# Optimization experiments

Measured on AMD Instinct MI355X. Metric: run time of the kernel, lower is better.

Reference implementation:

```python
import jax, jax.numpy as jnp
import numpy as np

N_HEAD = 12

def setup_inputs() -> dict:
    key = jax.random.key(0)
    k1, k2, k3, k4, k5 = jax.random.split(key, 5)
    B, T, C = 2, 2048, 768
    x = jax.random.normal(k1, (B, T, C), dtype=jnp.float32)
    W_attn = jax.random.normal(k2, (C, 3 * C), dtype=jnp.float32) * 0.02
    b_attn = jax.random.normal(k3, (3 * C,), dtype=jnp.float32) * 0.02
    W_proj = jax.random.normal(k4, (C, C), dtype=jnp.float32) * 0.02
    b_proj = jax.random.normal(k5, (C,), dtype=jnp.float32) * 0.02
    return {"x": x, "W_attn": W_attn, "b_attn": b_attn, "W_proj": W_proj, "b_proj": b_proj}

def reference(x, W_attn, b_attn, W_proj, b_proj):
    B, T, C = x.shape
    H = N_HEAD
    hd = C // H
    qkv = x @ W_attn + b_attn  # [B,T,3C]
    q, k, v = jnp.split(qkv, 3, axis=2)
    # [B,H,T,hd]
    q = q.reshape(B, T, H, hd).transpose(0, 2, 1, 3)
    k = k.reshape(B, T, H, hd).transpose(0, 2, 1, 3)
    v = v.reshape(B, T, H, hd).transpose(0, 2, 1, 3)
    att = jnp.einsum('bhqd,bhkd->bhqk', q, k) / jnp.sqrt(jnp.float32(hd))
    causal = jnp.tril(jnp.ones((T, T), dtype=bool))
    att = jnp.where(causal[None, None], att, -jnp.inf)
    att = jax.nn.softmax(att, axis=-1)
    y = jnp.einsum('bhqk,bhkd->bhqd', att, v)  # [B,H,T,hd]
    y = y.transpose(0, 2, 1, 3).reshape(B, T, C)
    return y @ W_proj + b_proj
```

## Files before the change

### kernel.cpp

```cpp
#include <hip/hip_runtime.h>
#include <stdint.h>

typedef unsigned short u16;
typedef __attribute__((ext_vector_type(8))) short bf16x8;
typedef __attribute__((ext_vector_type(4))) float f32x4;

__device__ __forceinline__ u16 f2bf(float f){
  union { float f; uint32_t u; } v; v.f = f;
  uint32_t u = v.u;
  u += 0x7FFFu + ((u >> 16) & 1u);
  return (u16)(u >> 16);
}

__device__ __forceinline__ float fexp2(float x){
#if __has_builtin(__builtin_amdgcn_exp2f)
  return __builtin_amdgcn_exp2f(x);
#else
  return exp2f(x);
#endif
}

__device__ __forceinline__ uint32_t cvtpk_bf16(float lo, float hi){
  uint32_t d;
  asm("v_cvt_pk_bf16_f32 %0, %1, %2" : "=v"(d) : "v"(lo), "v"(hi));
  return d;
}

__device__ __forceinline__ f32x4 mfma_bf16(bf16x8 a, bf16x8 b, f32x4 c){
  return __builtin_amdgcn_mfma_f32_16x16x32_bf16(a, b, c, 0, 0, 0);
}

#define GLOADX4(dst, off, sbase)                                            \
  asm volatile("global_load_dwordx4 %0, %1, %2"                             \
               : "=&v"(dst) : "v"(off), "s"(sbase))
#define GLOADX4_O64(dst, off, sbase)                                        \
  asm volatile("global_load_dwordx4 %0, %1, %2 offset:64"                   \
               : "=&v"(dst) : "v"(off), "s"(sbase))

#define QSCALE 0.1803368801111244f

__global__ __launch_bounds__(256) void cast_x_k(const float* __restrict__ x,
                                                u16* __restrict__ xb, int n4){
  int i = blockIdx.x*256 + threadIdx.x;
  if (i >= n4) return;
  float4 v = reinterpret_cast<const float4*>(x)[i];
  uint2 o;
  o.x = (uint32_t)f2bf(v.x) | ((uint32_t)f2bf(v.y) << 16);
  o.y = (uint32_t)f2bf(v.z) | ((uint32_t)f2bf(v.w) << 16);
  reinterpret_cast<uint2*>(xb)[i] = o;
}

__global__ __launch_bounds__(256) void transpose_cast_k(const float* __restrict__ in,
                                                        u16* __restrict__ out,
                                                        int R, int C){
  __shared__ u16 tile[64][66];
  int c0 = blockIdx.x*64, r0 = blockIdx.y*64;
  int tc = threadIdx.x & 63, t4 = threadIdx.x >> 6;
  #pragma unroll
  for (int i=0;i<16;i++){ int r = t4 + i*4; tile[r][tc] = f2bf(in[(size_t)(r0+r)*C + c0 + tc]); }
  __syncthreads();
  #pragma unroll
  for (int i=0;i<16;i++){ int cc = t4 + i*4; out[(size_t)(c0+cc)*R + r0 + tc] = tile[tc][cc]; }
}

#define LDP 40

__global__ __launch_bounds__(256) void gemm_bf16_k(
    const u16* __restrict__ A, const u16* __restrict__ Bt,
    int M, int N, int K, const float* __restrict__ bias, int mode,
    u16* __restrict__ qo, u16* __restrict__ ko, u16* __restrict__ vo,
    float* __restrict__ fo)
{
  __shared__ u16 As[128*LDP];
  __shared__ u16 Bs[128*LDP];
  const int m0 = blockIdx.y*128, n0 = blockIdx.x*128;
  const int tid = threadIdx.x, lane = tid & 63, wid = tid >> 6;
  const int lr = lane & 15, lg = lane >> 4;
  const int wr = wid >> 1, wc = wid & 1;
  f32x4 acc[4][4] = {};
  const int nk = K >> 5;
  for (int kk = 0; kk < nk; ++kk){
    #pragma unroll
    for (int s = 0; s < 2; ++s){
      int ci = tid + 256*s;
      int row = ci >> 2, ch = ci & 3;
      *(uint4*)&As[row*LDP + ch*8] = *(const uint4*)&A[(size_t)(m0+row)*K + kk*32 + ch*8];
      *(uint4*)&Bs[row*LDP + ch*8] = *(const uint4*)&Bt[(size_t)(n0+row)*K + kk*32 + ch*8];
    }
    __syncthreads();
    bf16x8 af[4], bfr[4];
    #pragma unroll
    for (int m=0;m<4;m++) af[m] = *(const bf16x8*)&As[(wr*64 + m*16 + lr)*LDP + lg*8];
    #pragma unroll
    for (int n=0;n<4;n++) bfr[n] = *(const bf16x8*)&Bs[(wc*64 + n*16 + lr)*LDP + lg*8];
    #pragma unroll
    for (int m=0;m<4;m++)
      #pragma unroll
      for (int n=0;n<4;n++)
        acc[m][n] = mfma_bf16(af[m], bfr[n], acc[m][n]);
    __syncthreads();
  }
  if (mode == 0){
    #pragma unroll
    for (int m=0;m<4;m++)
      #pragma unroll
      for (int n=0;n<4;n++){
        int gn = n0 + wc*64 + n*16 + lr;
        float bv = bias[gn];
        #pragma unroll
        for (int r=0;r<4;r++){
          int gm = m0 + wr*64 + m*16 + lg*4 + r;
          fo[(size_t)gm*N + gn] = acc[m][n][r] + bv;
        }
      }
  } else {
    int which = n0 / 768;
    u16* dst = (which==0) ? qo : ko;
    float sc = (which==0) ? QSCALE : 1.0f;
    #pragma unroll
    for (int m=0;m<4;m++)
      #pragma unroll
      for (int n=0;n<4;n++){
        int gn = n0 + wc*64 + n*16 + lr;
        float bv = bias[gn];
        int cn = gn - which*768;
        int h = cn >> 6, d = cn & 63;
        int gm0 = m0 + wr*64 + m*16 + lg*4;
        int b = gm0 >> 11, t0 = gm0 & 2047;
        if (which < 2){
          #pragma unroll
          for (int r=0;r<4;r++)
            dst[(size_t)((b*12 + h)*2048 + t0 + r)*64 + d] = f2bf((acc[m][n][r] + bv)*sc);
        } else {
          uint2 o;
          o.x = cvtpk_bf16(acc[m][n][0]+bv, acc[m][n][1]+bv);
          o.y = cvtpk_bf16(acc[m][n][2]+bv, acc[m][n][3]+bv);
          *(uint2*)&vo[((size_t)((b*12 + h)*64 + d))*2048 + t0] = o;
        }
      }
  }
}

__global__ __launch_bounds__(256) void attn_k(
    const u16* __restrict__ qp, const u16* __restrict__ kp,
    const u16* __restrict__ vtp, u16* __restrict__ yp)
{
  __shared__ f32x4 yl[2][16][64];
  __shared__ float ll[2][4][16];
  const int i = blockIdx.x;
  const int bh = i % 24;
  const int qb = 63 - (i / 24);
  const int q0 = qb * 32;
  const int q0A = q0, q0B = q0 + 16;
  const int b = bh / 12, h = bh - b*12;
  const size_t base = (size_t)bh * 131072;
  const int tid = threadIdx.x, lane = tid & 63, wid = tid >> 6;
  const int lr = lane & 15, lg = lane >> 4;
  const int qgA = q0A + lr, qgB = q0B + lr;
  const u16* kbase = kp + base;
  const u16* vbase = vtp + base;

  bf16x8 qfA[2], qfB[2];
  #pragma unroll
  for (int kb=0;kb<2;kb++){
    qfA[kb] = *(const bf16x8*)&qp[base + (size_t)qgA*64 + kb*32 + lg*8];
    qfB[kb] = *(const bf16x8*)&qp[base + (size_t)qgB*64 + kb*32 + lg*8];
  }

  f32x4 yA[4] = {}, yB[4] = {};
  float lA = 0.f, lB = 0.f;
  const float m2 = 8.f;
  const int nt = (qb >> 1) + 1;

  uint32_t ka0, ka1, ka2, ka3, va0, va1, va2, va3;
  {
    int p0 = ((0)*32 + (lr>>2)*8 + (0)*4 + (lr&3))*64 + lg*8;
    int p1 = ((1)*32 + (lr>>2)*8 + (0)*4 + (lr&3))*64 + lg*8;
    int p2 = ((0)*32 + (lr>>2)*8 + (1)*4 + (lr&3))*64 + lg*8;
    int p3 = ((1)*32 + (lr>>2)*8 + (1)*4 + (lr&3))*64 + lg*8;
    ka0 = (uint32_t)(wid*4096 + p0)*2u;  ka1 = (uint32_t)(wid*4096 + p1)*2u;
    ka2 = (uint32_t)(wid*4096 + p2)*2u;  ka3 = (uint32_t)(wid*4096 + p3)*2u;
    va0 = (uint32_t)((0*16+lr)*2048 + lg*8 + wid*64)*2u;
    va1 = (uint32_t)((1*16+lr)*2048 + lg*8 + wid*64)*2u;
    va2 = (uint32_t)((2*16+lr)*2048 + lg*8 + wid*64)*2u;
    va3 = (uint32_t)((3*16+lr)*2048 + lg*8 + wid*64)*2u;
  }

  bf16x8 kA[8], kB[8], vf[8];

  auto iter = [&](bf16x8 (&kc)[8], bf16x8 (&kn)[8], int t){
    asm volatile("s_waitcnt vmcnt(0)" ::: "memory");
    __builtin_amdgcn_sched_barrier(0);
    GLOADX4(vf[0], va0, vbase);  GLOADX4_O64(vf[1], va0, vbase);
    GLOADX4(vf[2], va1, vbase);  GLOADX4_O64(vf[3], va1, vbase);
    GLOADX4(vf[4], va2, vbase);  GLOADX4_O64(vf[5], va2, vbase);
    GLOADX4(vf[6], va3, vbase);  GLOADX4_O64(vf[7], va3, vbase);
    GLOADX4(kn[0], ka0, kbase);  GLOADX4_O64(kn[1], ka0, kbase);
    GLOADX4(kn[2], ka1, kbase);  GLOADX4_O64(kn[3], ka1, kbase);
    GLOADX4(kn[4], ka2, kbase);  GLOADX4_O64(kn[5], ka2, kbase);
    GLOADX4(kn[6], ka3, kbase);  GLOADX4_O64(kn[7], ka3, kbase);
    va0 += 512u; va1 += 512u; va2 += 512u; va3 += 512u;
    if (t + 8 < nt){ ka0 += 32768u; ka1 += 32768u; ka2 += 32768u; ka3 += 32768u; }

    const int k0 = t*64;
    const int nbmin[4] = {0, 32, 4, 36};
    uint32_t pkA[8], pkB[8];
    auto half_qk = [&](int q0H, int qgH, const bf16x8 (&qfH)[2],
                       float &lH, uint32_t (&pkH)[8]){
      f32x4 s[4] = {};
      __builtin_amdgcn_s_setprio(1);
      if (k0      <= q0H + 15){ s[0]=mfma_bf16(kc[0],qfH[0],s[0]); s[0]=mfma_bf16(kc[1],qfH[1],s[0]); }
      if (k0 + 32 <= q0H + 15){ s[1]=mfma_bf16(kc[2],qfH[0],s[1]); s[1]=mfma_bf16(kc[3],qfH[1],s[1]); }
      if (k0 +  4 <= q0H + 15){ s[2]=mfma_bf16(kc[4],qfH[0],s[2]); s[2]=mfma_bf16(kc[5],qfH[1],s[2]); }
      if (k0 + 36 <= q0H + 15){ s[3]=mfma_bf16(kc[6],qfH[0],s[3]); s[3]=mfma_bf16(kc[7],qfH[1],s[3]); }
      __builtin_amdgcn_s_setprio(0);
      if (k0 + 63 > q0H){
        #pragma unroll
        for (int nb=0;nb<4;nb++){
          int kb0 = k0 + (nb&1)*32 + ((nb>>1)&1)*4 + lg*8;
          #pragma unroll
          for (int r=0;r<4;r++)
            if (kb0 + r > qgH) s[nb][r] = -1e30f;
        }
      }
      float lsum = 0.f;
      #pragma unroll
      for (int nb=0;nb<4;nb++){
        if (k0 + nbmin[nb] <= q0H + 15){
          #pragma unroll
          for (int r=0;r<4;r++){
            float p = fexp2(s[nb][r] - m2);
            s[nb][r] = p;
            lsum += p;
          }
        } else {
          #pragma unroll
          for (int r=0;r<4;r++) s[nb][r] = 0.f;
        }
      }
      lH += lsum;
      #pragma unroll
      for (int nb=0;nb<4;nb++){
        pkH[nb*2]   = cvtpk_bf16(s[nb][0], s[nb][1]);
        pkH[nb*2+1] = cvtpk_bf16(s[nb][2], s[nb][3]);
      }
    };
    half_qk(q0A, qgA, qfA, lA, pkA);
    half_qk(q0B, qgB, qfB, lB, pkB);

    asm volatile("s_waitcnt vmcnt(8)" ::: "memory");
    __builtin_amdgcn_sched_barrier(0);
    __builtin_amdgcn_s_setprio(1);
    {
      union { uint32_t u[4]; bf16x8 v; } pb;
      pb.u[0]=pkA[0]; pb.u[1]=pkA[1]; pb.u[2]=pkA[4]; pb.u[3]=pkA[5];
      yA[0]=mfma_bf16(vf[0],pb.v,yA[0]); yA[1]=mfma_bf16(vf[2],pb.v,yA[1]);
      yA[2]=mfma_bf16(vf[4],pb.v,yA[2]); yA[3]=mfma_bf16(vf[6],pb.v,yA[3]);
      pb.u[0]=pkA[2]; pb.u[1]=pkA[3]; pb.u[2]=pkA[6]; pb.u[3]=pkA[7];
      yA[0]=mfma_bf16(vf[1],pb.v,yA[0]); yA[1]=mfma_bf16(vf[3],pb.v,yA[1]);
      yA[2]=mfma_bf16(vf[5],pb.v,yA[2]); yA[3]=mfma_bf16(vf[7],pb.v,yA[3]);
      pb.u[0]=pkB[0]; pb.u[1]=pkB[1]; pb.u[2]=pkB[4]; pb.u[3]=pkB[5];
      yB[0]=mfma_bf16(vf[0],pb.v,yB[0]); yB[1]=mfma_bf16(vf[2],pb.v,yB[1]);
      yB[2]=mfma_bf16(vf[4],pb.v,yB[2]); yB[3]=mfma_bf16(vf[6],pb.v,yB[3]);
      pb.u[0]=pkB[2]; pb.u[1]=pkB[3]; pb.u[2]=pkB[6]; pb.u[3]=pkB[7];
      yB[0]=mfma_bf16(vf[1],pb.v,yB[0]); yB[1]=mfma_bf16(vf[3],pb.v,yB[1]);
      yB[2]=mfma_bf16(vf[5],pb.v,yB[2]); yB[3]=mfma_bf16(vf[7],pb.v,yB[3]);
    }
    __builtin_amdgcn_s_setprio(0);
  };

  int t = wid;
  if (t < nt){
    GLOADX4(kA[0], ka0, kbase);  GLOADX4_O64(kA[1], ka0, kbase);
    GLOADX4(kA[2], ka1, kbase);  GLOADX4_O64(kA[3], ka1, kbase);
    GLOADX4(kA[4], ka2, kbase);  GLOADX4_O64(kA[5], ka2, kbase);
    GLOADX4(kA[6], ka3, kbase);  GLOADX4_O64(kA[7], ka3, kbase);
    if (t + 4 < nt){ ka0 += 32768u; ka1 += 32768u; ka2 += 32768u; ka3 += 32768u; }
    for (;;){
      iter(kA, kB, t);
      t += 4; if (t >= nt) break;
      iter(kB, kA, t);
      t += 4; if (t >= nt) break;
    }
  }

  lA += __shfl_xor(lA, 16);  lA += __shfl_xor(lA, 32);
  lB += __shfl_xor(lB, 16);  lB += __shfl_xor(lB, 32);

  #pragma unroll
  for (int n=0;n<4;n++){ yl[0][wid*4+n][lane] = yA[n]; yl[1][wid*4+n][lane] = yB[n]; }
  if (lg == 0){ ll[0][wid][lr] = lA; ll[1][wid][lr] = lB; }
  __syncthreads();

  #pragma unroll
  for (int hf=0; hf<2; hf++){
    float Ls = ll[hf][0][lr] + ll[hf][1][lr] + ll[hf][2][lr] + ll[hf][3][lr];
    f32x4 y0 = yl[hf][0*4+wid][lane], y1 = yl[hf][1*4+wid][lane],
          y2 = yl[hf][2*4+wid][lane], y3 = yl[hf][3*4+wid][lane];
    f32x4 ys;
    #pragma unroll
    for (int r=0;r<4;r++) ys[r] = (y0[r] + y1[r]) + (y2[r] + y3[r]);
    float inv = 1.0f / Ls;
    uint2 o;
    o.x = cvtpk_bf16(ys[0]*inv, ys[1]*inv);
    o.y = cvtpk_bf16(ys[2]*inv, ys[3]*inv);
    *(uint2*)&yp[(size_t)(b*2048 + q0 + hf*16 + lr)*768 + h*64 + wid*16 + lg*4] = o;
  }
}

extern "C" void kernel_launch(void* const* d_in, const int* in_sizes, int n_in,
                              void* d_out, int out_size, void* d_ws, size_t ws_size,
                              hipStream_t stream)
{
  const float* x  = (const float*)d_in[0];
  const float* Wa = (const float*)d_in[1];
  const float* ba = (const float*)d_in[2];
  const float* Wp = (const float*)d_in[3];
  const float* bp = (const float*)d_in[4];
  float* out = (float*)d_out;
  char* ws = (char*)d_ws;
  u16* xb  = (u16*)(ws + 0);
  u16* wt  = (u16*)(ws + 6291456);
  u16* wpt = (u16*)(ws + 9830400);
  u16* qb  = (u16*)(ws + 11010048);
  u16* kb  = (u16*)(ws + 17301504);
  u16* vtb = (u16*)(ws + 23592960);
  u16* yb  = (u16*)(ws + 29884416);

  cast_x_k<<<3072, 256, 0, stream>>>(x, xb, 786432);
  transpose_cast_k<<<dim3(36,12), 256, 0, stream>>>(Wa, wt, 768, 2304);
  transpose_cast_k<<<dim3(12,12), 256, 0, stream>>>(Wp, wpt, 768, 768);
  gemm_bf16_k<<<dim3(18,32), 256, 0, stream>>>(xb, wt, 4096, 2304, 768, ba, 1,
                                               qb, kb, vtb, nullptr);
  attn_k<<<1536, 256, 0, stream>>>(qb, kb, vtb, yb);
  gemm_bf16_k<<<dim3(6,32), 256, 0, stream>>>(yb, wpt, 4096, 768, 768, bp, 0,
                                              nullptr, nullptr, nullptr, out);
}
```

Measured before the change: 132.8 us.

## Replace hand-pipelined asm K/V loads with plain loads and halve LDS reduction buffer

The attention kernel drops the inline-asm global_load double-buffering of K tiles, with its manual vmcnt waits and sched barriers, in favour of a simple loop that issues plain vector loads of K and V each iteration and leaves scheduling to the compiler. The cross-wave reduction now reuses one half-sized LDS buffer for the two query halves in turn, with an extra barrier between them. This lowers LDS and register footprint, which may raise occupancy, but it gives up the explicit prefetch of the next K tile that overlapped memory latency with compute.

Measured after the change: 126.5 us. 1.05x faster.

```diff
diff --git a/kernel.cpp b/kernel.cpp
--- a/kernel.cpp
+++ b/kernel.cpp
@@ -29,13 +29,6 @@
 __device__ __forceinline__ f32x4 mfma_bf16(bf16x8 a, bf16x8 b, f32x4 c){
   return __builtin_amdgcn_mfma_f32_16x16x32_bf16(a, b, c, 0, 0, 0);
 }
-
-#define GLOADX4(dst, off, sbase)                                            \
-  asm volatile("global_load_dwordx4 %0, %1, %2"                             \
-               : "=&v"(dst) : "v"(off), "s"(sbase))
-#define GLOADX4_O64(dst, off, sbase)                                        \
-  asm volatile("global_load_dwordx4 %0, %1, %2 offset:64"                   \
-               : "=&v"(dst) : "v"(off), "s"(sbase))
 
 #define QSCALE 0.1803368801111244f
 
@@ -145,8 +138,8 @@
     const u16* __restrict__ qp, const u16* __restrict__ kp,
     const u16* __restrict__ vtp, u16* __restrict__ yp)
 {
-  __shared__ f32x4 yl[2][16][64];
-  __shared__ float ll[2][4][16];
+  __shared__ f32x4 ylh[16][64];
+  __shared__ float llh[4][16];
   const int i = blockIdx.x;
   const int bh = i % 24;
   const int qb = 63 - (i / 24);
@@ -172,47 +165,41 @@
   const float m2 = 8.f;
   const int nt = (qb >> 1) + 1;
 
-  uint32_t ka0, ka1, ka2, ka3, va0, va1, va2, va3;
-  {
-    int p0 = ((0)*32 + (lr>>2)*8 + (0)*4 + (lr&3))*64 + lg*8;
-    int p1 = ((1)*32 + (lr>>2)*8 + (0)*4 + (lr&3))*64 + lg*8;
-    int p2 = ((0)*32 + (lr>>2)*8 + (1)*4 + (lr&3))*64 + lg*8;
-    int p3 = ((1)*32 + (lr>>2)*8 + (1)*4 + (lr&3))*64 + lg*8;
-    ka0 = (uint32_t)(wid*4096 + p0)*2u;  ka1 = (uint32_t)(wid*4096 + p1)*2u;
-    ka2 = (uint32_t)(wid*4096 + p2)*2u;  ka3 = (uint32_t)(wid*4096 + p3)*2u;
-    va0 = (uint32_t)((0*16+lr)*2048 + lg*8 + wid*64)*2u;
-    va1 = (uint32_t)((1*16+lr)*2048 + lg*8 + wid*64)*2u;
-    va2 = (uint32_t)((2*16+lr)*2048 + lg*8 + wid*64)*2u;
-    va3 = (uint32_t)((3*16+lr)*2048 + lg*8 + wid*64)*2u;
-  }
-
-  bf16x8 kA[8], kB[8], vf[8];
-
-  auto iter = [&](bf16x8 (&kc)[8], bf16x8 (&kn)[8], int t){
-    asm volatile("s_waitcnt vmcnt(0)" ::: "memory");
-    __builtin_amdgcn_sched_barrier(0);
-    GLOADX4(vf[0], va0, vbase);  GLOADX4_O64(vf[1], va0, vbase);
-    GLOADX4(vf[2], va1, vbase);  GLOADX4_O64(vf[3], va1, vbase);
-    GLOADX4(vf[4], va2, vbase);  GLOADX4_O64(vf[5], va2, vbase);
-    GLOADX4(vf[6], va3, vbase);  GLOADX4_O64(vf[7], va3, vbase);
-    GLOADX4(kn[0], ka0, kbase);  GLOADX4_O64(kn[1], ka0, kbase);
-    GLOADX4(kn[2], ka1, kbase);  GLOADX4_O64(kn[3], ka1, kbase);
-    GLOADX4(kn[4], ka2, kbase);  GLOADX4_O64(kn[5], ka2, kbase);
-    GLOADX4(kn[6], ka3, kbase);  GLOADX4_O64(kn[7], ka3, kbase);
-    va0 += 512u; va1 += 512u; va2 += 512u; va3 += 512u;
-    if (t + 8 < nt){ ka0 += 32768u; ka1 += 32768u; ka2 += 32768u; ka3 += 32768u; }
+  uint32_t ko[8], vo[8];
+  #pragma unroll
+  for (int nb=0;nb<4;nb++){
+    int ke = ((nb&1)*32 + (lr>>2)*8 + (nb>>1)*4 + (lr&3))*64 + lg*8;
+    ko[nb*2+0] = (uint32_t)(wid*4096 + ke) * 2u;
+    ko[nb*2+1] = (uint32_t)(wid*4096 + ke + 32) * 2u;
+  }
+  #pragma unroll
+  for (int n=0;n<4;n++){
+    int ve = (n*16+lr)*2048 + lg*8 + wid*64;
+    vo[n*2+0] = (uint32_t)ve * 2u;
+    vo[n*2+1] = (uint32_t)(ve + 32) * 2u;
+  }
+
+  for (int t = wid; t < nt; t += 4){
+    bf16x8 kf[8], vf[8];
+    #pragma unroll
+    for (int j=0;j<8;j++) kf[j] = *(const bf16x8*)((const char*)kbase + ko[j]);
+    #pragma unroll
+    for (int j=0;j<8;j++) vf[j] = *(const bf16x8*)((const char*)vbase + vo[j]);
+    #pragma unroll
+    for (int j=0;j<8;j++){ ko[j] += 32768u; vo[j] += 512u; }
 
     const int k0 = t*64;
     const int nbmin[4] = {0, 32, 4, 36};
+
     uint32_t pkA[8], pkB[8];
     auto half_qk = [&](int q0H, int qgH, const bf16x8 (&qfH)[2],
                        float &lH, uint32_t (&pkH)[8]){
       f32x4 s[4] = {};
       __builtin_amdgcn_s_setprio(1);
-      if (k0      <= q0H + 15){ s[0]=mfma_bf16(kc[0],qfH[0],s[0]); s[0]=mfma_bf16(kc[1],qfH[1],s[0]); }
-      if (k0 + 32 <= q0H + 15){ s[1]=mfma_bf16(kc[2],qfH[0],s[1]); s[1]=mfma_bf16(kc[3],qfH[1],s[1]); }
-      if (k0 +  4 <= q0H + 15){ s[2]=mfma_bf16(kc[4],qfH[0],s[2]); s[2]=mfma_bf16(kc[5],qfH[1],s[2]); }
-      if (k0 + 36 <= q0H + 15){ s[3]=mfma_bf16(kc[6],qfH[0],s[3]); s[3]=mfma_bf16(kc[7],qfH[1],s[3]); }
+      if (k0      <= q0H + 15){ s[0]=mfma_bf16(kf[0],qfH[0],s[0]); s[0]=mfma_bf16(kf[1],qfH[1],s[0]); }
+      if (k0 + 32 <= q0H + 15){ s[1]=mfma_bf16(kf[2],qfH[0],s[1]); s[1]=mfma_bf16(kf[3],qfH[1],s[1]); }
+      if (k0 +  4 <= q0H + 15){ s[2]=mfma_bf16(kf[4],qfH[0],s[2]); s[2]=mfma_bf16(kf[5],qfH[1],s[2]); }
+      if (k0 + 36 <= q0H + 15){ s[3]=mfma_bf16(kf[6],qfH[0],s[3]); s[3]=mfma_bf16(kf[7],qfH[1],s[3]); }
       __builtin_amdgcn_s_setprio(0);
       if (k0 + 63 > q0H){
         #pragma unroll
@@ -248,8 +235,6 @@
     half_qk(q0A, qgA, qfA, lA, pkA);
     half_qk(q0B, qgB, qfB, lB, pkB);
 
-    asm volatile("s_waitcnt vmcnt(8)" ::: "memory");
-    __builtin_amdgcn_sched_barrier(0);
     __builtin_amdgcn_s_setprio(1);
     {
       union { uint32_t u[4]; bf16x8 v; } pb;
@@ -267,36 +252,21 @@
       yB[2]=mfma_bf16(vf[5],pb.v,yB[2]); yB[3]=mfma_bf16(vf[7],pb.v,yB[3]);
     }
     __builtin_amdgcn_s_setprio(0);
-  };
-
-  int t = wid;
-  if (t < nt){
-    GLOADX4(kA[0], ka0, kbase);  GLOADX4_O64(kA[1], ka0, kbase);
-    GLOADX4(kA[2], ka1, kbase);  GLOADX4_O64(kA[3], ka1, kbase);
-    GLOADX4(kA[4], ka2, kbase);  GLOADX4_O64(kA[5], ka2, kbase);
-    GLOADX4(kA[6], ka3, kbase);  GLOADX4_O64(kA[7], ka3, kbase);
-    if (t + 4 < nt){ ka0 += 32768u; ka1 += 32768u; ka2 += 32768u; ka3 += 32768u; }
-    for (;;){
-      iter(kA, kB, t);
-      t += 4; if (t >= nt) break;
-      iter(kB, kA, t);
-      t += 4; if (t >= nt) break;
-    }
   }
 
   lA += __shfl_xor(lA, 16);  lA += __shfl_xor(lA, 32);
   lB += __shfl_xor(lB, 16);  lB += __shfl_xor(lB, 32);
 
   #pragma unroll
-  for (int n=0;n<4;n++){ yl[0][wid*4+n][lane] = yA[n]; yl[1][wid*4+n][lane] = yB[n]; }
-  if (lg == 0){ ll[0][wid][lr] = lA; ll[1][wid][lr] = lB; }
-  __syncthreads();
-
-  #pragma unroll
   for (int hf=0; hf<2; hf++){
-    float Ls = ll[hf][0][lr] + ll[hf][1][lr] + ll[hf][2][lr] + ll[hf][3][lr];
-    f32x4 y0 = yl[hf][0*4+wid][lane], y1 = yl[hf][1*4+wid][lane],
-          y2 = yl[hf][2*4+wid][lane], y3 = yl[hf][3*4+wid][lane];
+    if (hf) __syncthreads();
+    #pragma unroll
+    for (int n=0;n<4;n++) ylh[wid*4+n][lane] = hf ? yB[n] : yA[n];
+    if (lg == 0) llh[wid][lr] = hf ? lB : lA;
+    __syncthreads();
+    float Ls = (llh[0][lr] + llh[1][lr]) + (llh[2][lr] + llh[3][lr]);
+    f32x4 y0 = ylh[0*4+wid][lane], y1 = ylh[1*4+wid][lane],
+          y2 = ylh[2*4+wid][lane], y3 = ylh[3*4+wid][lane];
     f32x4 ys;
     #pragma unroll
     for (int r=0;r<4;r++) ys[r] = (y0[r] + y1[r]) + (y2[r] + y3[r]);
```
